# Kernel optimization log

Measured on AMD Instinct MI355X. Metric: run time of the kernel, lower is better.

The kernel has to match this reference:

```python
import jax, jax.numpy as jnp
import numpy as np

N = 32768      # input points
P = 16         # num_points (kernel points == max neighbors per center)
NC = 8192      # centers after fps(ratio=0.25)
E = NC * P     # edges (exactly P neighbors per center, grouped by center)
IN_F = 64
OUT_F = 128
RADIUS = 1.0
KP_EXTENT = RADIUS / 1.5


def setup_inputs() -> dict:
    key = jax.random.key(0)
    k1, k2, k3, k4, k5 = jax.random.split(key, 5)
    x = jax.random.normal(k1, (N, IN_F), dtype=jnp.float32)
    pos = jax.random.normal(k2, (N, 3), dtype=jnp.float32)
    edge_src = jax.random.randint(k3, (E,), 0, N, dtype=jnp.int32)
    # edges grouped contiguously per center, P edges each (radius() output layout)
    edge_tgt = (jnp.arange(E, dtype=jnp.int32) // P)
    # kernel point positions inside the ball of radius KP-layout scale
    kernel_pts = jax.random.uniform(k4, (P, 3), dtype=jnp.float32,
                                    minval=-0.66 * RADIUS, maxval=0.66 * RADIUS)
    # kaiming-uniform-like init for [P, in, out] per-kernel-point weights
    bound = 1.0 / np.sqrt(IN_F)
    kernel_weight = jax.random.uniform(k5, (P, IN_F, OUT_F), dtype=jnp.float32,
                                       minval=-bound, maxval=bound)
    return {"x": x, "pos": pos, "edge_src": edge_src, "edge_tgt": edge_tgt,
            "kernel_pts": kernel_pts, "kernel_weight": kernel_weight}


def reference(x, pos, edge_src, edge_tgt, kernel_pts, kernel_weight):
    n_edges = edge_src.shape[0]
    nc = n_edges // P
    # gather endpoints (message_x_and_pos: pos_i, pos_j, x_j)
    pos_i = pos[edge_tgt]                       # [E,3]
    pos_j = pos[edge_src]                       # [E,3]
    rel = (pos_i - pos_j).reshape(nc, P, 3)     # neighbors, [NC,P,3]
    # distances from every neighbor to every kernel point
    diff = rel[:, :, None, :] - kernel_pts[None, None, :, :]   # [NC,P,K,3]
    sq = jnp.sum(diff * diff, axis=-1)                          # [NC,P,K]
    # linear KP influence, clamped at 0
    all_w = jnp.maximum(1.0 - jnp.sqrt(sq) / KP_EXTENT, 0.0)
    # one-hot argmin kernel assignment (VQ-like selection)
    nn_idx = jnp.argmin(sq, axis=-1)                            # [NC,P]
    one_hot = jax.nn.one_hot(nn_idx, P, dtype=all_w.dtype)      # [NC,P,K]
    all_w = all_w * one_hot
    feat = x[edge_src].reshape(nc, P, IN_F)                     # [NC,P,in]
    # weighted_features = all_w @ feat  (contract kernel axis vs neighbor axis)
    wf = jnp.einsum('cnk,cki->cni', all_w, feat)                # [NC,P,in]
    # per-edge matmul with the argmin-selected weight matrix; one_hot selects
    # W[nn_idx] without materializing the [E,in,out] gather
    msg = jnp.einsum('cni,cnk,kio->cno', wf, one_hot, kernel_weight)  # [NC,P,out]
    # scatter-add aggregation over target centers (MessagePassing aggr='add')
    out = jax.ops.segment_sum(msg.reshape(-1, OUT_F), edge_tgt, num_segments=NC)
    return out
```

## Files before the change

### kernel.cpp

```cpp
#include <hip/hip_runtime.h>
#include <hip/hip_bf16.h>


#define KPE 0.6666667f

typedef short short8 __attribute__((ext_vector_type(8)));
typedef float floatx4 __attribute__((ext_vector_type(4)));

__device__ inline unsigned short f2bf(float f) {
    __hip_bfloat16 h = __float2bfloat16(f);
    return __builtin_bit_cast(unsigned short, h);
}

__global__ __launch_bounds__(256) void kconv_prep(const float* __restrict__ Wf,
                                                  const float* __restrict__ x,
                                                  unsigned short* __restrict__ Wb,
                                                  unsigned short* __restrict__ xb) {
    const int t = threadIdx.x;
    if (blockIdx.x < 16) {
        const int m = blockIdx.x;
        __shared__ float tile[64 * 129];
#pragma unroll
        for (int j = 0; j < 32; ++j) {
            int idx = j * 256 + t;
            tile[(idx >> 7) * 129 + (idx & 127)] = Wf[m * 8192 + idx];
        }
        __syncthreads();
#pragma unroll
        for (int j = 0; j < 32; ++j) {
            int idx = j * 256 + t;
            Wb[m * 8192 + idx] = f2bf(tile[(idx & 63) * 129 + (idx >> 6)]);
        }
    } else {
        int idx4 = (blockIdx.x - 16) * 256 + t;
        const float4 v = reinterpret_cast<const float4*>(x)[idx4];
        ushort4 o;
        o.x = f2bf(v.x); o.y = f2bf(v.y); o.z = f2bf(v.z); o.w = f2bf(v.w);
        reinterpret_cast<ushort4*>(xb)[idx4] = o;
    }
}

__global__ __launch_bounds__(512) void kconv_main(
    const unsigned short* __restrict__ xb, const float* __restrict__ pos,
    const int* __restrict__ esrc, const int* __restrict__ etgt,
    const float* __restrict__ kpts, const unsigned short* __restrict__ Wb,
    float* __restrict__ out)
{
    __shared__ float kps[48];
    __shared__ float wv[32 * 17];
    __shared__ int   nnv[32 * 17];
    __shared__ int   srcv[16 * 32];
    __shared__ __align__(16) float s_loc[16 * 32];

    const int t = threadIdx.x;
    if (t < 48) kps[t] = kpts[t];

    const int e   = blockIdx.x * 512 + t;
    const int src = esrc[e];
    const int tgt = etgt[e];
    float rx = __fsub_rn(pos[tgt * 3 + 0], pos[src * 3 + 0]);
    float ry = __fsub_rn(pos[tgt * 3 + 1], pos[src * 3 + 1]);
    float rz = __fsub_rn(pos[tgt * 3 + 2], pos[src * 3 + 2]);
    __syncthreads();
    float best = 1e30f; int nn = 0;
#pragma unroll
    for (int k = 0; k < 16; ++k) {
        float dx = __fsub_rn(rx, kps[k * 3 + 0]);
        float dy = __fsub_rn(ry, kps[k * 3 + 1]);
        float dz = __fsub_rn(rz, kps[k * 3 + 2]);
        float sq = __fadd_rn(__fadd_rn(__fmul_rn(dx, dx), __fmul_rn(dy, dy)),
                             __fmul_rn(dz, dz));
        if (sq < best) { best = sq; nn = k; }
    }
    float w = fmaxf(__fsub_rn(1.0f, __fdiv_rn(__fsqrt_rn(best), KPE)), 0.0f);
    {
        const int r = t >> 4, n = t & 15;
        wv[r * 17 + n] = w; nnv[r * 17 + n] = nn;
        srcv[n * 32 + r] = src;
    }
    __syncthreads();

    {
        const int m = t >> 5, rr = t & 31;
        float sacc = 0.f;
#pragma unroll
        for (int n2 = 0; n2 < 16; ++n2)
            sacc += (nnv[rr * 17 + n2] == m) ? wv[rr * 17 + n2] : 0.f;
        s_loc[m * 32 + rr] = sacc;
    }
    __syncthreads();

    const uint4* xb4 = reinterpret_cast<const uint4*>(xb);
    const uint4* wb4 = reinterpret_cast<const uint4*>(Wb);
    const int wave = t >> 6, lane = t & 63;
    const int rg = wave & 1, cq = wave >> 2 ? (wave >> 1) & 3 : (wave >> 1) & 3;
    const int l16 = lane & 15, quad = lane >> 4;
    const int cqq = wave >> 1;
    const int arow = rg * 16 + l16;
    const int bq0 = (cqq * 32 + l16) * 8 + quad;
    const int bq1 = bq0 + 16 * 8;
    const int svoff = rg * 16 + quad * 4;

    uint4 A[2][2], B[2][4];
    float4 SV[2];
    {
        int s0 = srcv[arow];
        A[0][0] = xb4[s0 * 8 + quad];
        A[0][1] = xb4[s0 * 8 + 4 + quad];
        B[0][0] = wb4[bq0];
        B[0][1] = wb4[bq0 + 4];
        B[0][2] = wb4[bq1];
        B[0][3] = wb4[bq1 + 4];
        SV[0] = *reinterpret_cast<const float4*>(&s_loc[svoff]);
    }

    floatx4 acc0 = {0.f, 0.f, 0.f, 0.f};
    floatx4 acc1 = {0.f, 0.f, 0.f, 0.f};
    const floatx4 zed = {0.f, 0.f, 0.f, 0.f};

#pragma unroll
    for (int m = 0; m < 16; ++m) {
        const int cur = m & 1, nxt = cur ^ 1;
        if (m < 15) {
            int sn = srcv[(m + 1) * 32 + arow];
            A[nxt][0] = xb4[sn * 8 + quad];
            A[nxt][1] = xb4[sn * 8 + 4 + quad];
            const int wb = (m + 1) * 1024;
            B[nxt][0] = wb4[wb + bq0];
            B[nxt][1] = wb4[wb + bq0 + 4];
            B[nxt][2] = wb4[wb + bq1];
            B[nxt][3] = wb4[wb + bq1 + 4];
            SV[nxt] = *reinterpret_cast<const float4*>(&s_loc[(m + 1) * 32 + svoff]);
        }
        short8 a0 = __builtin_bit_cast(short8, A[cur][0]);
        short8 a1 = __builtin_bit_cast(short8, A[cur][1]);
        floatx4 t0 = __builtin_amdgcn_mfma_f32_16x16x32_bf16(
            a0, __builtin_bit_cast(short8, B[cur][0]), zed, 0, 0, 0);
        t0 = __builtin_amdgcn_mfma_f32_16x16x32_bf16(
            a1, __builtin_bit_cast(short8, B[cur][1]), t0, 0, 0, 0);
        floatx4 t1 = __builtin_amdgcn_mfma_f32_16x16x32_bf16(
            a0, __builtin_bit_cast(short8, B[cur][2]), zed, 0, 0, 0);
        t1 = __builtin_amdgcn_mfma_f32_16x16x32_bf16(
            a1, __builtin_bit_cast(short8, B[cur][3]), t1, 0, 0, 0);
        const float4 sv = SV[cur];
#pragma unroll
        for (int v = 0; v < 4; ++v) {
            const float s4 = (v == 0) ? sv.x : (v == 1) ? sv.y : (v == 2) ? sv.z : sv.w;
            acc0[v] += s4 * t0[v];
            acc1[v] += s4 * t1[v];
        }
    }

    const int col  = cqq * 32 + l16;
    const int row0 = blockIdx.x * 32 + rg * 16 + quad * 4;
#pragma unroll
    for (int v = 0; v < 4; ++v) {
        out[(row0 + v) * 128 + col]      = acc0[v];
        out[(row0 + v) * 128 + col + 16] = acc1[v];
    }
}

extern "C" void kernel_launch(void* const* d_in, const int* in_sizes, int n_in,
                              void* d_out, int out_size, void* d_ws, size_t ws_size,
                              hipStream_t stream) {
    const float* x    = (const float*)d_in[0];
    const float* pos  = (const float*)d_in[1];
    const int*   esrc = (const int*)d_in[2];
    const int*   etgt = (const int*)d_in[3];
    const float* kpts = (const float*)d_in[4];
    const float* Wf   = (const float*)d_in[5];
    float* out = (float*)d_out;

    char* wsb = (char*)d_ws;
    unsigned short* Wb = (unsigned short*)wsb;
    unsigned short* xb = (unsigned short*)(wsb + 262144);

    hipLaunchKernelGGL(kconv_prep, dim3(16 + 2048), dim3(256), 0, stream,
                       Wf, x, Wb, xb);
    hipLaunchKernelGGL(kconv_main, dim3(256), dim3(512), 0, stream,
                       xb, pos, esrc, etgt, kpts, Wb, out);
}
```

Measured before the change: 96.75 us.

## Move geometry to prep kernel and split kernel-point reduction across blocks with atomics

Result: no change. 97.81 us (+1.1%).

```diff
diff --git a/kernel.cpp b/kernel.cpp
--- a/kernel.cpp
+++ b/kernel.cpp
@@ -12,13 +12,49 @@
     return __builtin_bit_cast(unsigned short, h);
 }
 
-__global__ __launch_bounds__(256) void kconv_prep(const float* __restrict__ Wf,
-                                                  const float* __restrict__ x,
-                                                  unsigned short* __restrict__ Wb,
-                                                  unsigned short* __restrict__ xb) {
+__global__ __launch_bounds__(256) void kprep(
+    const float* __restrict__ Wf, const float* __restrict__ x,
+    const float* __restrict__ pos, const int* __restrict__ esrc,
+    const int* __restrict__ etgt, const float* __restrict__ kpts,
+    unsigned short* __restrict__ Wb, unsigned short* __restrict__ xb,
+    float* __restrict__ s_g, float* __restrict__ out)
+{
     const int t = threadIdx.x;
-    if (blockIdx.x < 16) {
-        const int m = blockIdx.x;
+    const int b = blockIdx.x;
+    if (b < 512) {
+        __shared__ float kps[48];
+        __shared__ float wv[16 * 17];
+        __shared__ int   nnv[16 * 17];
+        if (t < 48) kps[t] = kpts[t];
+        const int e   = b * 256 + t;
+        const int src = esrc[e];
+        const int tgt = etgt[e];
+        float rx = __fsub_rn(pos[tgt * 3 + 0], pos[src * 3 + 0]);
+        float ry = __fsub_rn(pos[tgt * 3 + 1], pos[src * 3 + 1]);
+        float rz = __fsub_rn(pos[tgt * 3 + 2], pos[src * 3 + 2]);
+        __syncthreads();
+        float best = 1e30f; int nn = 0;
+#pragma unroll
+        for (int k = 0; k < 16; ++k) {
+            float dx = __fsub_rn(rx, kps[k * 3 + 0]);
+            float dy = __fsub_rn(ry, kps[k * 3 + 1]);
+            float dz = __fsub_rn(rz, kps[k * 3 + 2]);
+            float sq = __fadd_rn(__fadd_rn(__fmul_rn(dx, dx), __fmul_rn(dy, dy)),
+                                 __fmul_rn(dz, dz));
+            if (sq < best) { best = sq; nn = k; }
+        }
+        float w = fmaxf(__fsub_rn(1.0f, __fdiv_rn(__fsqrt_rn(best), KPE)), 0.0f);
+        const int r = t >> 4, n = t & 15;
+        wv[r * 17 + n] = w; nnv[r * 17 + n] = nn;
+        __syncthreads();
+        const int mm = t >> 4, cl = t & 15;
+        float sacc = 0.f;
+#pragma unroll
+        for (int n2 = 0; n2 < 16; ++n2)
+            sacc += (nnv[cl * 17 + n2] == mm) ? wv[cl * 17 + n2] : 0.f;
+        s_g[mm * 8192 + b * 16 + cl] = sacc;
+    } else if (b < 528) {
+        const int m = b - 512;
         __shared__ float tile[64 * 129];
 #pragma unroll
         for (int j = 0; j < 32; ++j) {
@@ -31,132 +67,103 @@
             int idx = j * 256 + t;
             Wb[m * 8192 + idx] = f2bf(tile[(idx & 63) * 129 + (idx >> 6)]);
         }
+    } else if (b < 1040) {
+        const int base = (b - 528) * 1024;
+#pragma unroll
+        for (int j = 0; j < 4; ++j) {
+            int idx4 = base + j * 256 + t;
+            const float4 v = reinterpret_cast<const float4*>(x)[idx4];
+            ushort4 o;
+            o.x = f2bf(v.x); o.y = f2bf(v.y); o.z = f2bf(v.z); o.w = f2bf(v.w);
+            reinterpret_cast<ushort4*>(xb)[idx4] = o;
+        }
     } else {
-        int idx4 = (blockIdx.x - 16) * 256 + t;
-        const float4 v = reinterpret_cast<const float4*>(x)[idx4];
-        ushort4 o;
-        o.x = f2bf(v.x); o.y = f2bf(v.y); o.z = f2bf(v.z); o.w = f2bf(v.w);
-        reinterpret_cast<ushort4*>(xb)[idx4] = o;
+        const int base = (b - 1040) * 1024;
+        const float4 z = {0.f, 0.f, 0.f, 0.f};
+#pragma unroll
+        for (int j = 0; j < 4; ++j)
+            reinterpret_cast<float4*>(out)[base + j * 256 + t] = z;
     }
 }
 
-__global__ __launch_bounds__(512) void kconv_main(
-    const unsigned short* __restrict__ xb, const float* __restrict__ pos,
-    const int* __restrict__ esrc, const int* __restrict__ etgt,
-    const float* __restrict__ kpts, const unsigned short* __restrict__ Wb,
+__global__ __launch_bounds__(256) void kmain(
+    const unsigned short* __restrict__ xb, const int* __restrict__ esrc,
+    const unsigned short* __restrict__ Wb, const float* __restrict__ s_g,
     float* __restrict__ out)
 {
-    __shared__ float kps[48];
-    __shared__ float wv[32 * 17];
-    __shared__ int   nnv[32 * 17];
-    __shared__ int   srcv[16 * 32];
-    __shared__ __align__(16) float s_loc[16 * 32];
-
-    const int t = threadIdx.x;
-    if (t < 48) kps[t] = kpts[t];
-
-    const int e   = blockIdx.x * 512 + t;
-    const int src = esrc[e];
-    const int tgt = etgt[e];
-    float rx = __fsub_rn(pos[tgt * 3 + 0], pos[src * 3 + 0]);
-    float ry = __fsub_rn(pos[tgt * 3 + 1], pos[src * 3 + 1]);
-    float rz = __fsub_rn(pos[tgt * 3 + 2], pos[src * 3 + 2]);
-    __syncthreads();
-    float best = 1e30f; int nn = 0;
-#pragma unroll
-    for (int k = 0; k < 16; ++k) {
-        float dx = __fsub_rn(rx, kps[k * 3 + 0]);
-        float dy = __fsub_rn(ry, kps[k * 3 + 1]);
-        float dz = __fsub_rn(rz, kps[k * 3 + 2]);
-        float sq = __fadd_rn(__fadd_rn(__fmul_rn(dx, dx), __fmul_rn(dy, dy)),
-                             __fmul_rn(dz, dz));
-        if (sq < best) { best = sq; nn = k; }
-    }
-    float w = fmaxf(__fsub_rn(1.0f, __fdiv_rn(__fsqrt_rn(best), KPE)), 0.0f);
-    {
-        const int r = t >> 4, n = t & 15;
-        wv[r * 17 + n] = w; nnv[r * 17 + n] = nn;
-        srcv[n * 32 + r] = src;
-    }
-    __syncthreads();
-
-    {
-        const int m = t >> 5, rr = t & 31;
-        float sacc = 0.f;
-#pragma unroll
-        for (int n2 = 0; n2 < 16; ++n2)
-            sacc += (nnv[rr * 17 + n2] == m) ? wv[rr * 17 + n2] : 0.f;
-        s_loc[m * 32 + rr] = sacc;
-    }
-    __syncthreads();
-
     const uint4* xb4 = reinterpret_cast<const uint4*>(xb);
     const uint4* wb4 = reinterpret_cast<const uint4*>(Wb);
-    const int wave = t >> 6, lane = t & 63;
-    const int rg = wave & 1, cq = wave >> 2 ? (wave >> 1) & 3 : (wave >> 1) & 3;
-    const int l16 = lane & 15, quad = lane >> 4;
-    const int cqq = wave >> 1;
-    const int arow = rg * 16 + l16;
-    const int bq0 = (cqq * 32 + l16) * 8 + quad;
-    const int bq1 = bq0 + 16 * 8;
-    const int svoff = rg * 16 + quad * 4;
+    const int t    = threadIdx.x;
+    const int w    = t >> 6, lane = t & 63;
+    const int l16  = lane & 15, quad = lane >> 4;
+    const int rt   = blockIdx.x >> 1, ks = blockIdx.x & 1;
+    const int r0   = rt * 16;
+    const int m0   = ks * 8;
+    const int bc0  = (w * 32 + l16) * 8 + quad;
+    const int bc1  = (w * 32 + 16 + l16) * 8 + quad;
+    const int srcbase = (r0 + l16) * 16 + m0;
+    const int svbase  = r0 + quad * 4;
 
-    uint4 A[2][2], B[2][4];
+    int srcv[8];
+#pragma unroll
+    for (int i = 0; i < 8; ++i) srcv[i] = esrc[srcbase + i];
+
+    uint4  A[3][2];
+    uint4  B[2][4];
     float4 SV[2];
-    {
-        int s0 = srcv[arow];
-        A[0][0] = xb4[s0 * 8 + quad];
-        A[0][1] = xb4[s0 * 8 + 4 + quad];
-        B[0][0] = wb4[bq0];
-        B[0][1] = wb4[bq0 + 4];
-        B[0][2] = wb4[bq1];
-        B[0][3] = wb4[bq1 + 4];
-        SV[0] = *reinterpret_cast<const float4*>(&s_loc[svoff]);
-    }
+
+    A[0][0] = xb4[srcv[0] * 8 + quad];  A[0][1] = xb4[srcv[0] * 8 + 4 + quad];
+    A[1][0] = xb4[srcv[1] * 8 + quad];  A[1][1] = xb4[srcv[1] * 8 + 4 + quad];
+    B[0][0] = wb4[m0 * 1024 + bc0];     B[0][1] = wb4[m0 * 1024 + bc0 + 4];
+    B[0][2] = wb4[m0 * 1024 + bc1];     B[0][3] = wb4[m0 * 1024 + bc1 + 4];
+    SV[0]   = *reinterpret_cast<const float4*>(&s_g[m0 * 8192 + svbase]);
 
     floatx4 acc0 = {0.f, 0.f, 0.f, 0.f};
     floatx4 acc1 = {0.f, 0.f, 0.f, 0.f};
     const floatx4 zed = {0.f, 0.f, 0.f, 0.f};
 
 #pragma unroll
-    for (int m = 0; m < 16; ++m) {
-        const int cur = m & 1, nxt = cur ^ 1;
-        if (m < 15) {
-            int sn = srcv[(m + 1) * 32 + arow];
-            A[nxt][0] = xb4[sn * 8 + quad];
-            A[nxt][1] = xb4[sn * 8 + 4 + quad];
-            const int wb = (m + 1) * 1024;
-            B[nxt][0] = wb4[wb + bq0];
-            B[nxt][1] = wb4[wb + bq0 + 4];
-            B[nxt][2] = wb4[wb + bq1];
-            B[nxt][3] = wb4[wb + bq1 + 4];
-            SV[nxt] = *reinterpret_cast<const float4*>(&s_loc[(m + 1) * 32 + svoff]);
+    for (int i = 0; i < 8; ++i) {
+        if (i + 2 < 8) {
+            const int s2 = srcv[i + 2];
+            A[(i + 2) % 3][0] = xb4[s2 * 8 + quad];
+            A[(i + 2) % 3][1] = xb4[s2 * 8 + 4 + quad];
         }
-        short8 a0 = __builtin_bit_cast(short8, A[cur][0]);
-        short8 a1 = __builtin_bit_cast(short8, A[cur][1]);
+        if (i + 1 < 8) {
+            const int mb = (m0 + i + 1) * 1024;
+            B[(i + 1) & 1][0] = wb4[mb + bc0];
+            B[(i + 1) & 1][1] = wb4[mb + bc0 + 4];
+            B[(i + 1) & 1][2] = wb4[mb + bc1];
+            B[(i + 1) & 1][3] = wb4[mb + bc1 + 4];
+            SV[(i + 1) & 1] = *reinterpret_cast<const float4*>(
+                &s_g[(m0 + i + 1) * 8192 + svbase]);
+        }
+        const short8 a0 = __builtin_bit_cast(short8, A[i % 3][0]);
+        const short8 a1 = __builtin_bit_cast(short8, A[i % 3][1]);
         floatx4 t0 = __builtin_amdgcn_mfma_f32_16x16x32_bf16(
-            a0, __builtin_bit_cast(short8, B[cur][0]), zed, 0, 0, 0);
+            a0, __builtin_bit_cast(short8, B[i & 1][0]), zed, 0, 0, 0);
         t0 = __builtin_amdgcn_mfma_f32_16x16x32_bf16(
-            a1, __builtin_bit_cast(short8, B[cur][1]), t0, 0, 0, 0);
+            a1, __builtin_bit_cast(short8, B[i & 1][1]), t0, 0, 0, 0);
         floatx4 t1 = __builtin_amdgcn_mfma_f32_16x16x32_bf16(
-            a0, __builtin_bit_cast(short8, B[cur][2]), zed, 0, 0, 0);
+            a0, __builtin_bit_cast(short8, B[i & 1][2]), zed, 0, 0, 0);
         t1 = __builtin_amdgcn_mfma_f32_16x16x32_bf16(
-            a1, __builtin_bit_cast(short8, B[cur][3]), t1, 0, 0, 0);
-        const float4 sv = SV[cur];
+            a1, __builtin_bit_cast(short8, B[i & 1][3]), t1, 0, 0, 0);
+        const float4 sv = SV[i & 1];
 #pragma unroll
         for (int v = 0; v < 4; ++v) {
-            const float s4 = (v == 0) ? sv.x : (v == 1) ? sv.y : (v == 2) ? sv.z : sv.w;
+            const float s4 = (v == 0) ? sv.x : (v == 1) ? sv.y
+                           : (v == 2) ? sv.z : sv.w;
             acc0[v] += s4 * t0[v];
             acc1[v] += s4 * t1[v];
         }
     }
 
-    const int col  = cqq * 32 + l16;
-    const int row0 = blockIdx.x * 32 + rg * 16 + quad * 4;
+    const int col0 = w * 32 + l16;
+    const int rowb = r0 + quad * 4;
 #pragma unroll
     for (int v = 0; v < 4; ++v) {
-        out[(row0 + v) * 128 + col]      = acc0[v];
-        out[(row0 + v) * 128 + col + 16] = acc1[v];
+        atomicAdd(&out[(rowb + v) * 128 + col0],      acc0[v]);
+        atomicAdd(&out[(rowb + v) * 128 + col0 + 16], acc1[v]);
     }
 }
 
@@ -174,9 +181,10 @@
     char* wsb = (char*)d_ws;
     unsigned short* Wb = (unsigned short*)wsb;
     unsigned short* xb = (unsigned short*)(wsb + 262144);
+    float*          sg = (float*)(wsb + 262144 + 4194304);
 
-    hipLaunchKernelGGL(kconv_prep, dim3(16 + 2048), dim3(256), 0, stream,
-                       Wf, x, Wb, xb);
-    hipLaunchKernelGGL(kconv_main, dim3(256), dim3(512), 0, stream,
-                       xb, pos, esrc, etgt, kpts, Wb, out);
+    hipLaunchKernelGGL(kprep, dim3(1296), dim3(256), 0, stream,
+                       Wf, x, pos, esrc, etgt, kpts, Wb, xb, sg, out);
+    hipLaunchKernelGGL(kmain, dim3(1024), dim3(256), 0, stream,
+                       xb, esrc, Wb, sg, out);
 }
```

## Drop x bf16 prepass; gather fp32 x directly and convert in main kernel

Applied to the files above, without the earlier changes.

Result: slower. 102.0 us (+5.4%).

```diff
diff --git a/kernel.cpp b/kernel.cpp
--- a/kernel.cpp
+++ b/kernel.cpp
@@ -12,50 +12,49 @@
     return __builtin_bit_cast(unsigned short, h);
 }
 
-__global__ __launch_bounds__(256) void kconv_prep(const float* __restrict__ Wf,
-                                                  const float* __restrict__ x,
-                                                  unsigned short* __restrict__ Wb,
-                                                  unsigned short* __restrict__ xb) {
+__device__ inline short8 pack8(float4 u, float4 v) {
+    short8 r;
+    r[0] = (short)f2bf(u.x); r[1] = (short)f2bf(u.y);
+    r[2] = (short)f2bf(u.z); r[3] = (short)f2bf(u.w);
+    r[4] = (short)f2bf(v.x); r[5] = (short)f2bf(v.y);
+    r[6] = (short)f2bf(v.z); r[7] = (short)f2bf(v.w);
+    return r;
+}
+
+__global__ __launch_bounds__(256) void kw(const float* __restrict__ Wf,
+                                          unsigned short* __restrict__ Wb) {
     const int t = threadIdx.x;
-    if (blockIdx.x < 16) {
-        const int m = blockIdx.x;
-        __shared__ float tile[64 * 129];
+    const int m = blockIdx.x;
+    __shared__ float tile[64 * 129];
 #pragma unroll
-        for (int j = 0; j < 32; ++j) {
-            int idx = j * 256 + t;
-            tile[(idx >> 7) * 129 + (idx & 127)] = Wf[m * 8192 + idx];
-        }
-        __syncthreads();
+    for (int j = 0; j < 32; ++j) {
+        int idx = j * 256 + t;
+        tile[(idx >> 7) * 129 + (idx & 127)] = Wf[m * 8192 + idx];
+    }
+    __syncthreads();
 #pragma unroll
-        for (int j = 0; j < 32; ++j) {
-            int idx = j * 256 + t;
-            Wb[m * 8192 + idx] = f2bf(tile[(idx & 63) * 129 + (idx >> 6)]);
-        }
-    } else {
-        int idx4 = (blockIdx.x - 16) * 256 + t;
-        const float4 v = reinterpret_cast<const float4*>(x)[idx4];
-        ushort4 o;
-        o.x = f2bf(v.x); o.y = f2bf(v.y); o.z = f2bf(v.z); o.w = f2bf(v.w);
-        reinterpret_cast<ushort4*>(xb)[idx4] = o;
+    for (int j = 0; j < 32; ++j) {
+        int idx = j * 256 + t;
+        Wb[m * 8192 + idx] = f2bf(tile[(idx & 63) * 129 + (idx >> 6)]);
     }
 }
 
-__global__ __launch_bounds__(512) void kconv_main(
-    const unsigned short* __restrict__ xb, const float* __restrict__ pos,
+__global__ __launch_bounds__(256, 2) void kmain(
+    const float* __restrict__ x, const float* __restrict__ pos,
     const int* __restrict__ esrc, const int* __restrict__ etgt,
     const float* __restrict__ kpts, const unsigned short* __restrict__ Wb,
     float* __restrict__ out)
 {
     __shared__ float kps[48];
-    __shared__ float wv[32 * 17];
-    __shared__ int   nnv[32 * 17];
-    __shared__ int   srcv[16 * 32];
-    __shared__ __align__(16) float s_loc[16 * 32];
+    __shared__ float wv[16 * 17];
+    __shared__ int   nnv[16 * 17];
+    __shared__ __align__(16) int   srcv[16 * 16];
+    __shared__ __align__(16) float s_loc[16 * 16];
 
     const int t = threadIdx.x;
     if (t < 48) kps[t] = kpts[t];
 
-    const int e   = blockIdx.x * 512 + t;
+    const int e   = blockIdx.x * 256 + t;
     const int src = esrc[e];
     const int tgt = etgt[e];
     float rx = __fsub_rn(pos[tgt * 3 + 0], pos[src * 3 + 0]);
@@ -76,83 +75,91 @@
     {
         const int r = t >> 4, n = t & 15;
         wv[r * 17 + n] = w; nnv[r * 17 + n] = nn;
-        srcv[n * 32 + r] = src;
+        srcv[r * 16 + n] = src;
+    }
+    __syncthreads();
+    {
+        const int mm = t >> 4, cl = t & 15;
+        float sacc = 0.f;
+#pragma unroll
+        for (int n2 = 0; n2 < 16; ++n2)
+            sacc += (nnv[cl * 17 + n2] == mm) ? wv[cl * 17 + n2] : 0.f;
+        s_loc[mm * 16 + cl] = sacc;
     }
     __syncthreads();
 
+    const float4* x4f = reinterpret_cast<const float4*>(x);
+    const uint4*  wb4 = reinterpret_cast<const uint4*>(Wb);
+    const int wv_ = t >> 6, lane = t & 63;
+    const int l16 = lane & 15, quad = lane >> 4;
+    const int bc0 = (wv_ * 32 + l16) * 8 + quad;
+    const int bc1 = bc0 + 128;
+
+    int sidx[16];
     {
-        const int m = t >> 5, rr = t & 31;
-        float sacc = 0.f;
+        const int4* sp = reinterpret_cast<const int4*>(&srcv[l16 * 16]);
+        int4 q0 = sp[0], q1 = sp[1], q2 = sp[2], q3 = sp[3];
+        sidx[0]=q0.x; sidx[1]=q0.y; sidx[2]=q0.z;  sidx[3]=q0.w;
+        sidx[4]=q1.x; sidx[5]=q1.y; sidx[6]=q1.z;  sidx[7]=q1.w;
+        sidx[8]=q2.x; sidx[9]=q2.y; sidx[10]=q2.z; sidx[11]=q2.w;
+        sidx[12]=q3.x; sidx[13]=q3.y; sidx[14]=q3.z; sidx[15]=q3.w;
+    }
+
+    float4 A[3][4];
+    uint4  B[2][4];
+    float4 SV[2];
+    const int aq = quad * 2;
 #pragma unroll
-        for (int n2 = 0; n2 < 16; ++n2)
-            sacc += (nnv[rr * 17 + n2] == m) ? wv[rr * 17 + n2] : 0.f;
-        s_loc[m * 32 + rr] = sacc;
+    for (int p = 0; p < 2; ++p) {
+        const int sr = sidx[p] * 16;
+        A[p][0] = x4f[sr + aq];     A[p][1] = x4f[sr + aq + 1];
+        A[p][2] = x4f[sr + 8 + aq]; A[p][3] = x4f[sr + 8 + aq + 1];
     }
-    __syncthreads();
-
-    const uint4* xb4 = reinterpret_cast<const uint4*>(xb);
-    const uint4* wb4 = reinterpret_cast<const uint4*>(Wb);
-    const int wave = t >> 6, lane = t & 63;
-    const int rg = wave & 1, cq = wave >> 2 ? (wave >> 1) & 3 : (wave >> 1) & 3;
-    const int l16 = lane & 15, quad = lane >> 4;
-    const int cqq = wave >> 1;
-    const int arow = rg * 16 + l16;
-    const int bq0 = (cqq * 32 + l16) * 8 + quad;
-    const int bq1 = bq0 + 16 * 8;
-    const int svoff = rg * 16 + quad * 4;
-
-    uint4 A[2][2], B[2][4];
-    float4 SV[2];
-    {
-        int s0 = srcv[arow];
-        A[0][0] = xb4[s0 * 8 + quad];
-        A[0][1] = xb4[s0 * 8 + 4 + quad];
-        B[0][0] = wb4[bq0];
-        B[0][1] = wb4[bq0 + 4];
-        B[0][2] = wb4[bq1];
-        B[0][3] = wb4[bq1 + 4];
-        SV[0] = *reinterpret_cast<const float4*>(&s_loc[svoff]);
-    }
+    B[0][0] = wb4[bc0]; B[0][1] = wb4[bc0 + 4];
+    B[0][2] = wb4[bc1]; B[0][3] = wb4[bc1 + 4];
+    SV[0] = *reinterpret_cast<const float4*>(&s_loc[quad * 4]);
 
     floatx4 acc0 = {0.f, 0.f, 0.f, 0.f};
     floatx4 acc1 = {0.f, 0.f, 0.f, 0.f};
     const floatx4 zed = {0.f, 0.f, 0.f, 0.f};
 
 #pragma unroll
-    for (int m = 0; m < 16; ++m) {
-        const int cur = m & 1, nxt = cur ^ 1;
-        if (m < 15) {
-            int sn = srcv[(m + 1) * 32 + arow];
-            A[nxt][0] = xb4[sn * 8 + quad];
-            A[nxt][1] = xb4[sn * 8 + 4 + quad];
-            const int wb = (m + 1) * 1024;
-            B[nxt][0] = wb4[wb + bq0];
-            B[nxt][1] = wb4[wb + bq0 + 4];
-            B[nxt][2] = wb4[wb + bq1];
-            B[nxt][3] = wb4[wb + bq1 + 4];
-            SV[nxt] = *reinterpret_cast<const float4*>(&s_loc[(m + 1) * 32 + svoff]);
+    for (int i = 0; i < 16; ++i) {
+        const int cur = i % 3, bcur = i & 1;
+        if (i + 2 < 16) {
+            const int sr = sidx[i + 2] * 16, slot = (i + 2) % 3;
+            A[slot][0] = x4f[sr + aq];     A[slot][1] = x4f[sr + aq + 1];
+            A[slot][2] = x4f[sr + 8 + aq]; A[slot][3] = x4f[sr + 8 + aq + 1];
         }
-        short8 a0 = __builtin_bit_cast(short8, A[cur][0]);
-        short8 a1 = __builtin_bit_cast(short8, A[cur][1]);
+        if (i + 1 < 16) {
+            const int mb = (i + 1) * 1024, bn = bcur ^ 1;
+            B[bn][0] = wb4[mb + bc0]; B[bn][1] = wb4[mb + bc0 + 4];
+            B[bn][2] = wb4[mb + bc1]; B[bn][3] = wb4[mb + bc1 + 4];
+            SV[bn] = *reinterpret_cast<const float4*>(
+                &s_loc[(i + 1) * 16 + quad * 4]);
+        }
+        const short8 a0 = pack8(A[cur][0], A[cur][1]);
+        const short8 a1 = pack8(A[cur][2], A[cur][3]);
         floatx4 t0 = __builtin_amdgcn_mfma_f32_16x16x32_bf16(
-            a0, __builtin_bit_cast(short8, B[cur][0]), zed, 0, 0, 0);
+            a0, __builtin_bit_cast(short8, B[bcur][0]), zed, 0, 0, 0);
         t0 = __builtin_amdgcn_mfma_f32_16x16x32_bf16(
-            a1, __builtin_bit_cast(short8, B[cur][1]), t0, 0, 0, 0);
+            a1, __builtin_bit_cast(short8, B[bcur][1]), t0, 0, 0, 0);
         floatx4 t1 = __builtin_amdgcn_mfma_f32_16x16x32_bf16(
-            a0, __builtin_bit_cast(short8, B[cur][2]), zed, 0, 0, 0);
+            a0, __builtin_bit_cast(short8, B[bcur][2]), zed, 0, 0, 0);
         t1 = __builtin_amdgcn_mfma_f32_16x16x32_bf16(
-            a1, __builtin_bit_cast(short8, B[cur][3]), t1, 0, 0, 0);
-        const float4 sv = SV[cur];
+            a1, __builtin_bit_cast(short8, B[bcur][3]), t1, 0, 0, 0);
+        const float4 sv = SV[bcur];
 #pragma unroll
         for (int v = 0; v < 4; ++v) {
-            const float s4 = (v == 0) ? sv.x : (v == 1) ? sv.y : (v == 2) ? sv.z : sv.w;
+            const float s4 = (v == 0) ? sv.x : (v == 1) ? sv.y
+                           : (v == 2) ? sv.z : sv.w;
             acc0[v] += s4 * t0[v];
             acc1[v] += s4 * t1[v];
         }
     }
 
-    const int col  = cqq * 32 + l16;
-    const int row0 = blockIdx.x * 32 + rg * 16 + quad * 4;
+    const int col  = wv_ * 32 + l16;
+    const int row0 = blockIdx.x * 16 + quad * 4;
 #pragma unroll
     for (int v = 0; v < 4; ++v) {
         out[(row0 + v) * 128 + col]      = acc0[v];
@@ -170,13 +177,9 @@
     const float* kpts = (const float*)d_in[4];
     const float* Wf   = (const float*)d_in[5];
     float* out = (float*)d_out;
+    unsigned short* Wb = (unsigned short*)d_ws;
 
-    char* wsb = (char*)d_ws;
-    unsigned short* Wb = (unsigned short*)wsb;
-    unsigned short* xb = (unsigned short*)(wsb + 262144);
-
-    hipLaunchKernelGGL(kconv_prep, dim3(16 + 2048), dim3(256), 0, stream,
-                       Wf, x, Wb, xb);
-    hipLaunchKernelGGL(kconv_main, dim3(256), dim3(512), 0, stream,
-                       xb, pos, esrc, etgt, kpts, Wb, out);
+    hipLaunchKernelGGL(kw,    dim3(16),  dim3(256), 0, stream, Wf, Wb);
+    hipLaunchKernelGGL(kmain, dim3(512), dim3(256), 0, stream,
+                       x, pos, esrc, etgt, kpts, Wb, out);
 }
```
